# Optimization experiments

Measured on AMD Instinct MI355X. Metric: run time of the kernel, lower is better.

## Reference

```python
import jax, jax.numpy as jnp
import numpy as np

N_NODES = 100000
N_EDGES = 1600000
IN_DIM = 64
OUT_DIM = 64


def setup_inputs() -> dict:
    key = jax.random.key(0)
    k1, k2, k3, k4, k5, k6 = jax.random.split(key, 6)
    # xavier-uniform-ish scales for the linear weights (gain=1.414)
    fc_bound = 1.414 * np.sqrt(6.0 / (IN_DIM + OUT_DIM))
    at_bound = 1.414 * np.sqrt(6.0 / (OUT_DIM + 1))
    return {
        "h_src": jax.random.normal(k1, (N_NODES, IN_DIM), dtype=jnp.float32),
        "h_dst": jax.random.normal(k2, (N_NODES, IN_DIM), dtype=jnp.float32),
        "W_fc": jax.random.uniform(k3, (OUT_DIM, IN_DIM), dtype=jnp.float32,
                                   minval=-fc_bound, maxval=fc_bound),
        "w_attn": jax.random.uniform(k4, (OUT_DIM,), dtype=jnp.float32,
                                     minval=-at_bound, maxval=at_bound),
        "src": jax.random.randint(k5, (N_EDGES,), 0, N_NODES, dtype=jnp.int64),
        "dst": jnp.sort(jax.random.randint(k6, (N_EDGES,), 0, N_NODES, dtype=jnp.int64)),
    }


def reference(h_src, h_dst, W_fc, w_attn, src, dst):
    # Per-edge feature difference: dst - src  (edge_attention)
    diff_e = h_dst[dst] - h_src[src]                      # [E, in_dim]
    # fc projection (dropout p=0 in eval) then attention score
    d = diff_e @ W_fc.T                                   # [E, out_dim]
    e = jnp.tanh(d @ w_attn)                              # [E]
    # Segment softmax over incoming edges of each destination node
    m = jax.ops.segment_max(e, dst, num_segments=N_NODES)  # [N], -inf for empty
    ex = jnp.exp(e - m[dst])                              # [E]
    s = jax.ops.segment_sum(ex, dst, num_segments=N_NODES)  # [N]
    alpha = ex / s[dst]                                   # [E]
    # Weighted sum aggregation of projected diffs per destination node
    h_diff = jax.ops.segment_sum(alpha[:, None] * d, dst, num_segments=N_NODES)  # [N, out_dim]
    return jax.nn.elu(h_diff)
```

## Files before the change

kernel.cpp:

```cpp
#include <hip/hip_runtime.h>
#include <hip/hip_fp16.h>
#include <math.h>

#define NN 100000
#define NE 1600000
#define DIM 64

__device__ __forceinline__ __half2 u2h2(unsigned u) { __half2 h; __builtin_memcpy(&h, &u, 4); return h; }
__device__ __forceinline__ unsigned h22u(__half2 h) { unsigned u; __builtin_memcpy(&u, &h, 4); return u; }
__device__ __forceinline__ unsigned pk_f16(float a, float b) {
    auto h = __builtin_amdgcn_cvt_pkrtz(a, b);
    unsigned u; __builtin_memcpy(&u, &h, 4); return u;
}

#define WS 68

__global__ __launch_bounds__(256) void proj_kernel(
    const float* __restrict__ h_src, const float* __restrict__ h_dst,
    const float* __restrict__ W, const float* __restrict__ w_attn,
    unsigned* __restrict__ p16, float* __restrict__ a_src, float* __restrict__ a_dst) {
    __shared__ __align__(16) float Wt[DIM * WS];
    __shared__ __align__(16) float Ht[DIM * WS];
    __shared__ __align__(16) float was[DIM];

    const int t = threadIdx.x;
    const int row0 = blockIdx.x * 64;

#pragma unroll
    for (int r = 0; r < 16; ++r) {
        int idx = r * 256 + t;
        int j = idx >> 6, k = idx & 63;
        Wt[k * WS + j] = W[idx];
    }
    if (t < DIM) was[t] = w_attn[t];

    {
        int k = t & 63;
        int nb = t >> 6;
#pragma unroll
        for (int r = 0; r < 16; ++r) {
            int nl = r * 4 + nb;
            int row = row0 + nl;
            const float* hp = (row < NN) ? (h_src + (size_t)row * DIM)
                                         : (h_dst + (size_t)(row - NN) * DIM);
            Ht[k * WS + nl] = hp[k];
        }
    }
    __syncthreads();

    const int jg = (t & 15) * 4;
    const int ng = (t >> 4) * 4;
    float acc[4][4];
#pragma unroll
    for (int a = 0; a < 4; ++a)
#pragma unroll
        for (int b = 0; b < 4; ++b) acc[a][b] = 0.f;

#pragma unroll 4
    for (int k = 0; k < DIM; ++k) {
        const float4 wv = *(const float4*)(Wt + k * WS + jg);
        const float4 hv = *(const float4*)(Ht + k * WS + ng);
        const float wa[4] = {wv.x, wv.y, wv.z, wv.w};
        const float ha[4] = {hv.x, hv.y, hv.z, hv.w};
#pragma unroll
        for (int a = 0; a < 4; ++a)
#pragma unroll
            for (int b = 0; b < 4; ++b) acc[a][b] += ha[a] * wa[b];
    }

    const float4 wat4 = *(const float4*)(was + jg);
#pragma unroll
    for (int a = 0; a < 4; ++a) {
        int row = row0 + ng + a;
        uint2 pk;
        pk.x = pk_f16(acc[a][0], acc[a][1]);
        pk.y = pk_f16(acc[a][2], acc[a][3]);
        *(uint2*)(p16 + (size_t)row * 32 + (jg >> 1)) = pk;

        float pa = acc[a][0] * wat4.x + acc[a][1] * wat4.y +
                   acc[a][2] * wat4.z + acc[a][3] * wat4.w;
#pragma unroll
        for (int off = 8; off; off >>= 1) pa += __shfl_xor(pa, off);
        if ((t & 15) == 0) {
            if (row < NN) a_src[row] = pa;
            else a_dst[row - NN] = pa;
        }
    }
}

__global__ void rowptr_kernel(const int* __restrict__ dst, int* __restrict__ row_ptr) {
    int i = blockIdx.x * blockDim.x + threadIdx.x;
    if (i >= NE) return;
    int d = dst[i];
    int prev = (i == 0) ? -1 : dst[i - 1];
    for (int n = prev + 1; n <= d; ++n) row_ptr[n] = i;
    if (i == NE - 1) {
        for (int n = d + 1; n <= NN; ++n) row_ptr[n] = NE;
    }
}

__global__ __launch_bounds__(256) void agg_kernel(
    const char* __restrict__ p16base,
    const float* __restrict__ a_src, const float* __restrict__ a_dst,
    const int* __restrict__ src, const int* __restrict__ row_ptr,
    float4* __restrict__ out4) {
    __shared__ uint2 buf[4][64];
    const int wv = threadIdx.x >> 6;
    const int lane = threadIdx.x & 63;
    const int wid = blockIdx.x * 4 + wv;
    if (wid >= NN) return;

    const int sub = lane >> 3;
    const int chunk = lane & 7;
    const size_t ob = (size_t)wid * 16 + chunk * 2;

    const int beg = row_ptr[wid];
    const int end = row_ptr[wid + 1];

    if (end <= beg) {
        if (sub == 0) {
            out4[ob]     = make_float4(0.f, 0.f, 0.f, 0.f);
            out4[ob + 1] = make_float4(0.f, 0.f, 0.f, 0.f);
        }
        return;
    }

    const float ad = a_dst[wid];
    const char* pbase = p16base + (size_t)chunk * 16;

    float sAcc = 0.f;
    __half2 acc[4];
#pragma unroll
    for (int q = 0; q < 4; ++q) acc[q] = u2h2(0u);

    uint2* bufw = buf[wv];

    for (int cb = beg; cb < end; cb += 64) {
        int cd = end - cb; if (cd > 64) cd = 64;
        uint2 pk = make_uint2(0u, 0u);
        if (lane < cd) {
            int sv = src[cb + lane];
            float x = ad - a_src[sv];
            float th = 1.f - 2.f / (__expf(2.f * x) + 1.f);
            float w = __expf(th);
            sAcc += w;
            pk.x = pk_f16(w, w);
            pk.y = (unsigned)sv * 128u;
        }
        bufw[lane] = pk;

        for (int j = 0; j < cd; j += 16) {
            uint2 e0 = bufw[j + sub];
            uint2 e1 = bufw[j + 8 + sub];
            uint4 r0 = *(const uint4*)(pbase + e0.y);
            uint4 r1 = *(const uint4*)(pbase + e1.y);
            __half2 w0 = u2h2(e0.x), w1 = u2h2(e1.x);
            acc[0] = __hfma2(w0, u2h2(r0.x), acc[0]);
            acc[1] = __hfma2(w0, u2h2(r0.y), acc[1]);
            acc[2] = __hfma2(w0, u2h2(r0.z), acc[2]);
            acc[3] = __hfma2(w0, u2h2(r0.w), acc[3]);
            acc[0] = __hfma2(w1, u2h2(r1.x), acc[0]);
            acc[1] = __hfma2(w1, u2h2(r1.y), acc[1]);
            acc[2] = __hfma2(w1, u2h2(r1.z), acc[2]);
            acc[3] = __hfma2(w1, u2h2(r1.w), acc[3]);
        }
    }

#pragma unroll
    for (int off = 32; off; off >>= 1) sAcc += __shfl_xor(sAcc, off);
#pragma unroll
    for (int off = 8; off <= 32; off <<= 1) {
#pragma unroll
        for (int q = 0; q < 4; ++q)
            acc[q] = __hadd2(acc[q], u2h2(__shfl_xor(h22u(acc[q]), off)));
    }

    if (sub == 0) {
        const uint4 pdu = *(const uint4*)(p16base + ((size_t)(NN + wid)) * 128 + (size_t)chunk * 16);
        const unsigned pw[4] = {pdu.x, pdu.y, pdu.z, pdu.w};
        const float inv = 1.f / sAcc;
        float o[8];
#pragma unroll
        for (int q = 0; q < 4; ++q) {
            float2 pf = __half22float2(u2h2(pw[q]));
            float2 af = __half22float2(acc[q]);
            float h0 = pf.x - af.x * inv;
            float h1 = pf.y - af.y * inv;
            o[2 * q]     = h0 > 0.f ? h0 : __expf(h0) - 1.f;
            o[2 * q + 1] = h1 > 0.f ? h1 : __expf(h1) - 1.f;
        }
        out4[ob]     = make_float4(o[0], o[1], o[2], o[3]);
        out4[ob + 1] = make_float4(o[4], o[5], o[6], o[7]);
    }
}

extern "C" void kernel_launch(void* const* d_in, const int* in_sizes, int n_in,
                              void* d_out, int out_size, void* d_ws, size_t ws_size,
                              hipStream_t stream) {
    const float* h_src = (const float*)d_in[0];
    const float* h_dst = (const float*)d_in[1];
    const float* W     = (const float*)d_in[2];
    const float* w_at  = (const float*)d_in[3];
    const int*   src   = (const int*)d_in[4];
    const int*   dst   = (const int*)d_in[5];

    char* ws = (char*)d_ws;
    unsigned* p16 = (unsigned*)ws;
    float* a_src = (float*)(ws + (size_t)2 * NN * 32 * 4);
    float* a_dst = a_src + NN;
    int* row_ptr = (int*)(a_dst + NN);

    hipLaunchKernelGGL(proj_kernel, dim3((2 * NN) / 64), dim3(256), 0, stream,
                       h_src, h_dst, W, w_at, p16, a_src, a_dst);
    hipLaunchKernelGGL(rowptr_kernel, dim3((NE + 255) / 256), dim3(256), 0, stream,
                       dst, row_ptr);
    hipLaunchKernelGGL(agg_kernel, dim3((NN + 3) / 4), dim3(256), 0, stream,
                       (const char*)p16, a_src, a_dst, src, row_ptr,
                       (float4*)d_out);
}
```

Baseline: 176.0 us.

## Process four destination nodes per wavefront with 16-lane groups in aggregation

```diff
diff --git a/kernel.cpp b/kernel.cpp
--- a/kernel.cpp
+++ b/kernel.cpp
@@ -107,51 +107,46 @@
     __shared__ uint2 buf[4][64];
     const int wv = threadIdx.x >> 6;
     const int lane = threadIdx.x & 63;
-    const int wid = blockIdx.x * 4 + wv;
+    const int g = lane >> 4;
+    const int glane = lane & 15;
+    const int sub16 = glane >> 3;
+    const int chunk = glane & 7;
+
+    const int wid = (blockIdx.x * 4 + wv) * 4 + g;
     if (wid >= NN) return;
-
-    const int sub = lane >> 3;
-    const int chunk = lane & 7;
-    const size_t ob = (size_t)wid * 16 + chunk * 2;
 
     const int beg = row_ptr[wid];
     const int end = row_ptr[wid + 1];
-
-    if (end <= beg) {
-        if (sub == 0) {
-            out4[ob]     = make_float4(0.f, 0.f, 0.f, 0.f);
-            out4[ob + 1] = make_float4(0.f, 0.f, 0.f, 0.f);
-        }
-        return;
-    }
-
-    const float ad = a_dst[wid];
+    const bool nonempty = end > beg;
+
+    const float ad = nonempty ? a_dst[wid] : 0.f;
     const char* pbase = p16base + (size_t)chunk * 16;
+    uint2* bufw = buf[wv];
+    const int gbase = g * 16;
 
     float sAcc = 0.f;
     __half2 acc[4];
 #pragma unroll
     for (int q = 0; q < 4; ++q) acc[q] = u2h2(0u);
 
-    uint2* bufw = buf[wv];
-
-    for (int cb = beg; cb < end; cb += 64) {
-        int cd = end - cb; if (cd > 64) cd = 64;
+    for (int cb = beg; cb < end; cb += 16) {
+        int cd = end - cb; if (cd > 16) cd = 16;
         uint2 pk = make_uint2(0u, 0u);
-        if (lane < cd) {
-            int sv = src[cb + lane];
+        float w = 0.f;
+        if (glane < cd) {
+            int sv = src[cb + glane];
             float x = ad - a_src[sv];
             float th = 1.f - 2.f / (__expf(2.f * x) + 1.f);
-            float w = __expf(th);
-            sAcc += w;
+            w = __expf(th);
             pk.x = pk_f16(w, w);
             pk.y = (unsigned)sv * 128u;
         }
+        sAcc += w;
         bufw[lane] = pk;
 
-        for (int j = 0; j < cd; j += 16) {
-            uint2 e0 = bufw[j + sub];
-            uint2 e1 = bufw[j + 8 + sub];
+        for (int j = 0; j < cd; j += 4) {
+            uint2 e0 = bufw[gbase + j + sub16];
+            uint2 e1 = bufw[gbase + j + 2 + sub16];
             uint4 r0 = *(const uint4*)(pbase + e0.y);
             uint4 r1 = *(const uint4*)(pbase + e1.y);
             __half2 w0 = u2h2(e0.x), w1 = u2h2(e1.x);
@@ -167,28 +162,26 @@
     }
 
 #pragma unroll
-    for (int off = 32; off; off >>= 1) sAcc += __shfl_xor(sAcc, off);
-#pragma unroll
-    for (int off = 8; off <= 32; off <<= 1) {
-#pragma unroll
-        for (int q = 0; q < 4; ++q)
-            acc[q] = __hadd2(acc[q], u2h2(__shfl_xor(h22u(acc[q]), off)));
-    }
-
-    if (sub == 0) {
+    for (int off = 1; off <= 8; off <<= 1) sAcc += __shfl_xor(sAcc, off);
+#pragma unroll
+    for (int q = 0; q < 4; ++q)
+        acc[q] = __hadd2(acc[q], u2h2(__shfl_xor(h22u(acc[q]), 8)));
+
+    if (sub16 == 0) {
         const uint4 pdu = *(const uint4*)(p16base + ((size_t)(NN + wid)) * 128 + (size_t)chunk * 16);
         const unsigned pw[4] = {pdu.x, pdu.y, pdu.z, pdu.w};
-        const float inv = 1.f / sAcc;
+        const float inv = nonempty ? 1.f / sAcc : 0.f;
         float o[8];
 #pragma unroll
         for (int q = 0; q < 4; ++q) {
             float2 pf = __half22float2(u2h2(pw[q]));
             float2 af = __half22float2(acc[q]);
-            float h0 = pf.x - af.x * inv;
-            float h1 = pf.y - af.y * inv;
+            float h0 = nonempty ? (pf.x - af.x * inv) : 0.f;
+            float h1 = nonempty ? (pf.y - af.y * inv) : 0.f;
             o[2 * q]     = h0 > 0.f ? h0 : __expf(h0) - 1.f;
             o[2 * q + 1] = h1 > 0.f ? h1 : __expf(h1) - 1.f;
         }
+        const size_t ob = (size_t)wid * 16 + chunk * 2;
         out4[ob]     = make_float4(o[0], o[1], o[2], o[3]);
         out4[ob + 1] = make_float4(o[4], o[5], o[6], o[7]);
     }
@@ -214,7 +207,7 @@
                        h_src, h_dst, W, w_at, p16, a_src, a_dst);
     hipLaunchKernelGGL(rowptr_kernel, dim3((NE + 255) / 256), dim3(256), 0, stream,
                        dst, row_ptr);
-    hipLaunchKernelGGL(agg_kernel, dim3((NN + 3) / 4), dim3(256), 0, stream,
+    hipLaunchKernelGGL(agg_kernel, dim3((NN + 15) / 16), dim3(256), 0, stream,
                        (const char*)p16, a_src, a_dst, src, row_ptr,
                        (float4*)d_out);
 }
```

After: 164.7 us. 6.4% less time.
